# Performance work log

Measured on AMD Instinct MI355X. Metric: run time of the kernel, lower is better.

## Reference

```python
import jax, jax.numpy as jnp
import numpy as np

OUT, IN = 4096, 4096
GROUP_SIZE = 64
NUM_GROUPS = IN // GROUP_SIZE  # 64


def dequantize(packed, mn, scale):
    # packed: [OUT, NUM_GROUPS, GROUP_SIZE//2] int32, byte values 0..255.
    # 4-bit asymmetric layout (torch compress): high nibble holds the first
    # half of each group, low nibble the second half.
    hi = (packed >> 4) & 0xF                      # [OUT, G, 32]
    lo = packed & 0xF                             # [OUT, G, 32]
    vals = jnp.concatenate([hi, lo], axis=-1).astype(jnp.float32)  # [OUT, G, 64]
    w = vals / scale + mn                         # scale, mn broadcast [OUT, G, 1]
    return w.reshape(OUT, IN)


def setup_inputs() -> dict:
    key = jax.random.key(0)
    k1, k2, k3, k4, k5 = jax.random.split(key, 5)
    x = jax.random.normal(k1, (4, 2048, IN), dtype=jnp.float32)
    packed = jax.random.randint(k2, (OUT, NUM_GROUPS, GROUP_SIZE // 2), 0, 256, dtype=jnp.int32)
    mn = jax.random.normal(k3, (OUT, NUM_GROUPS, 1), dtype=jnp.float32) * 0.02
    # scale = B / (mx - mn) is positive; keep it away from zero.
    scale = jax.random.uniform(k4, (OUT, NUM_GROUPS, 1), dtype=jnp.float32) * 200.0 + 100.0
    bias = jax.random.normal(k5, (OUT,), dtype=jnp.float32) * 0.02
    return {"x": x, "packed": packed, "mn": mn, "scale": scale, "bias": bias}


def reference(x, packed, mn, scale, bias):
    w = dequantize(packed, mn, scale)             # [OUT, IN] fp32
    # F.linear: out = x @ w.T + bias
    return jnp.einsum('bsk,nk->bsn', x, w) + bias
```

## Files before the change

kernel.cpp:

```cpp
#include <hip/hip_runtime.h>

typedef unsigned short u16;
typedef unsigned int u32;
typedef _Float16 f16;
typedef f16 f16x2 __attribute__((ext_vector_type(2)));
typedef f16 f16x8 __attribute__((ext_vector_type(8)));
typedef __fp16 h16x2 __attribute__((ext_vector_type(2)));
typedef float f32x4 __attribute__((ext_vector_type(4)));

#define M_DIM 8192
#define N_DIM 4096
#define K_DIM 4096

#define XCVT_BLOCKS 16384
#define W4_BLOCKS 8192
#define IM_BLOCKS 1024

__global__ __launch_bounds__(256) void prep_kernel(
    const float4* __restrict__ x, uint4* __restrict__ xh,
    const int* __restrict__ packed, u32* __restrict__ w4,
    const float* __restrict__ mn, const float* __restrict__ scale,
    uint2* __restrict__ invmn) {
  int b = blockIdx.x;
  if (b < XCVT_BLOCKS) {
    int i = b * 256 + threadIdx.x;
    float4 a0 = x[2 * i], a1 = x[2 * i + 1];
    h16x2 h0 = __builtin_amdgcn_cvt_pkrtz(a0.x, a0.y);
    h16x2 h1 = __builtin_amdgcn_cvt_pkrtz(a0.z, a0.w);
    h16x2 h2 = __builtin_amdgcn_cvt_pkrtz(a1.x, a1.y);
    h16x2 h3 = __builtin_amdgcn_cvt_pkrtz(a1.z, a1.w);
    uint4 o;
    o.x = __builtin_bit_cast(u32, h0);
    o.y = __builtin_bit_cast(u32, h1);
    o.z = __builtin_bit_cast(u32, h2);
    o.w = __builtin_bit_cast(u32, h3);
    xh[i] = o;
  } else if (b < XCVT_BLOCKS + W4_BLOCKS) {
    int idx = (b - XCVT_BLOCKS) * 256 + threadIdx.x;
    int n = idx >> 9, w = idx & 511;
    int g = w >> 3;
    int jb = (w & 7) << 3;
    int sh = (jb < 32) ? 4 : 0;
    const int* p = packed + n * 2048 + g * 32 + (jb & 31);
    u32 out = 0;
#pragma unroll
    for (int t = 0; t < 8; t++) {
      u32 nib = ((u32)p[t] >> sh) & 0xFu;
      int pos = ((t & 1) ? 16 : 0) + ((t >> 1) << 2);
      out |= nib << pos;
    }
    w4[idx] = out;
  } else {
    int idx = (b - XCVT_BLOCKS - W4_BLOCKS) * 256 + threadIdx.x;
    int n = idx & 4095, g = idx >> 12;
    float sc = scale[n * 64 + g];
    float m = mn[n * 64 + g];
    f16 invh = (f16)(1.0f / sc);
    f16 mnh = (f16)(m - 16.0f * (float)invh);
    u32 ib = (u32)__builtin_bit_cast(u16, invh);
    u32 mb = (u32)__builtin_bit_cast(u16, mnh);
    uint2 o;
    o.x = ib | (ib << 16);
    o.y = mb | (mb << 16);
    invmn[idx] = o;
  }
}

__device__ __forceinline__ void gload_lds16(const void* g, void* l) {
  __builtin_amdgcn_global_load_lds(
      (const __attribute__((address_space(1))) void*)g,
      (__attribute__((address_space(3))) void*)l, 16, 0, 0);
}

__global__ __launch_bounds__(256, 2) void gemm4_kernel(
    const u16* __restrict__ A,
    const u32* __restrict__ B4,
    const uint2* __restrict__ IM,
    const float* __restrict__ bias, float* __restrict__ C) {
  __shared__ alignas(16) u16 As[2][256 * 32];
  __shared__ alignas(16) u32 Bs[2][128 * 4];

  const int tid = threadIdx.x;
  const int wave = tid >> 6, lane = tid & 63;
  const int lr = lane & 15, lq = lane >> 4;
  const int bn = blockIdx.x & 31, bm = blockIdx.x >> 5;
  const int m0 = bm << 8, n0 = bn << 7;
  const int wm = (wave & 1) << 7, wn = (wave >> 1) << 6;

  const u16* pA =
      A + (size_t)(m0 + (wave << 6) + (lane >> 2)) * K_DIM + ((lane & 3) << 3);
  char* dstA = (char*)(&As[0][0]) + wave * 4096 + lane * 16;
  const u32* pB = B4 + (size_t)(n0 + ((wave & 1) << 6) + lane) * 512 +
                  ((wave >> 1) << 2);
  char* dstB = (char*)(&Bs[0][0]) + wave * 1024 + lane * 16;
  const uint2* pI = IM + n0 + wn + lr;

  f32x4 acc[8][4] = {};

  for (int kk = 0; kk < 64; ++kk) {
    uint2 im[4];
    const uint2* pIt = pI + kk * 4096;
#pragma unroll
    for (int j = 0; j < 4; j++) im[j] = pIt[j * 16];

#pragma unroll
    for (int s = 0; s < 2; s++)
#pragma unroll
      for (int c = 0; c < 4; c++)
        gload_lds16(pA + kk * 64 + s * 32 + (size_t)c * 16 * K_DIM,
                    dstA + s * 16384 + c * 1024);
    gload_lds16(pB + kk * 8, dstB);
    __syncthreads();

#pragma unroll
    for (int s = 0; s < 2; s++) {
      f16x8 af[8];
#pragma unroll
      for (int i = 0; i < 8; i++)
        af[i] = *(const f16x8*)((const char*)(&As[0][0]) + s * 16384 +
                                (wm + i * 16 + lr) * 64 + lq * 16);
      u32 braw[4];
#pragma unroll
      for (int j = 0; j < 4; j++) braw[j] = Bs[s][(wn + j * 16 + lr) * 4 + lq];

      f16x8 bf[4];
#pragma unroll
      for (int j = 0; j < 4; j++) {
        u32 d = braw[j];
        u32 q0 = ((d << 6) & 0x03C003C0u) | 0x4C004C00u;
        u32 q1 = ((d << 2) & 0x03C003C0u) | 0x4C004C00u;
        u32 q2 = ((d >> 2) & 0x03C003C0u) | 0x4C004C00u;
        u32 q3 = ((d >> 6) & 0x03C003C0u) | 0x4C004C00u;
        f16x2 inv2 = __builtin_bit_cast(f16x2, im[j].x);
        f16x2 mn2 = __builtin_bit_cast(f16x2, im[j].y);
        f16x2 w0 = __builtin_elementwise_fma(__builtin_bit_cast(f16x2, q0), inv2, mn2);
        f16x2 w1 = __builtin_elementwise_fma(__builtin_bit_cast(f16x2, q1), inv2, mn2);
        f16x2 w2 = __builtin_elementwise_fma(__builtin_bit_cast(f16x2, q2), inv2, mn2);
        f16x2 w3 = __builtin_elementwise_fma(__builtin_bit_cast(f16x2, q3), inv2, mn2);
        union {
          f16x8 v;
          u32 d[4];
        } u;
        u.d[0] = __builtin_bit_cast(u32, w0);
        u.d[1] = __builtin_bit_cast(u32, w1);
        u.d[2] = __builtin_bit_cast(u32, w2);
        u.d[3] = __builtin_bit_cast(u32, w3);
        bf[j] = u.v;
      }
#pragma unroll
      for (int i = 0; i < 8; i++)
#pragma unroll
        for (int j = 0; j < 4; j++)
          acc[i][j] = __builtin_amdgcn_mfma_f32_16x16x32_f16(af[i], bf[j],
                                                             acc[i][j], 0, 0, 0);
    }
    __syncthreads();
  }

#pragma unroll
  for (int j = 0; j < 4; j++) {
    int n = n0 + wn + j * 16 + lr;
    float bv = bias[n];
#pragma unroll
    for (int i = 0; i < 8; i++) {
      int mb = m0 + wm + i * 16 + (lq << 2);
#pragma unroll
      for (int t = 0; t < 4; t++)
        C[(size_t)(mb + t) * N_DIM + n] = acc[i][j][t] + bv;
    }
  }
}

__global__ __launch_bounds__(256) void fallback_gemm(
    const float* __restrict__ x, const int* __restrict__ packed,
    const float* __restrict__ mn, const float* __restrict__ scale,
    const float* __restrict__ bias, float* __restrict__ out) {
  __shared__ float As[16][17];
  __shared__ float Bs[16][17];
  int tx = threadIdx.x & 15, ty = threadIdx.x >> 4;
  int m = blockIdx.y * 16 + ty;
  int n = blockIdx.x * 16 + tx;
  float acc = 0.f;
  for (int k0 = 0; k0 < K_DIM; k0 += 16) {
    As[ty][tx] = x[(size_t)m * K_DIM + k0 + tx];
    int nn = blockIdx.x * 16 + ty;
    int k = k0 + tx;
    int g = k >> 6, pos = k & 63;
    int p = packed[nn * 2048 + g * 32 + (pos & 31)];
    int v = (pos < 32) ? ((p >> 4) & 0xF) : (p & 0xF);
    Bs[ty][tx] = (float)v / scale[nn * 64 + g] + mn[nn * 64 + g];
    __syncthreads();
#pragma unroll
    for (int kk = 0; kk < 16; kk++) acc += As[ty][kk] * Bs[tx][kk];
    __syncthreads();
  }
  out[(size_t)m * N_DIM + n] = acc + bias[n];
}

extern "C" void kernel_launch(void* const* d_in, const int* in_sizes, int n_in,
                              void* d_out, int out_size, void* d_ws,
                              size_t ws_size, hipStream_t stream) {
  const float* x = (const float*)d_in[0];
  const int* packed = (const int*)d_in[1];
  const float* mn = (const float*)d_in[2];
  const float* scale = (const float*)d_in[3];
  const float* bias = (const float*)d_in[4];
  float* out = (float*)d_out;

  const size_t offW4 = (size_t)M_DIM * K_DIM * 2;
  const size_t offIM = offW4 + (size_t)N_DIM * K_DIM / 2;
  const size_t need = offIM + (size_t)64 * N_DIM * 8;

  if (ws_size >= need) {
    u16* Xh = (u16*)d_ws;
    u32* W4 = (u32*)((char*)d_ws + offW4);
    uint2* IMp = (uint2*)((char*)d_ws + offIM);
    prep_kernel<<<XCVT_BLOCKS + W4_BLOCKS + IM_BLOCKS, 256, 0, stream>>>(
        (const float4*)x, (uint4*)Xh, packed, W4, mn, scale, IMp);
    gemm4_kernel<<<(M_DIM / 256) * (N_DIM / 128), 256, 0, stream>>>(
        Xh, W4, IMp, bias, out);
  } else {
    dim3 grid(N_DIM / 16, M_DIM / 16);
    fallback_gemm<<<grid, 256, 0, stream>>>(x, packed, mn, scale, bias, out);
  }
}
```

Measured before the change: 515.8 us.

## Double-buffer LDS tiles with prefetch and XOR-swizzle A layout

Converts the GEMM main loop to a double-buffered scheme: the next K-slice of A, B and the scale/min pairs is loaded into the alternate LDS buffer while the current one feeds MFMAs, leaving one barrier per iteration. It also XOR-swizzles the 16-byte chunks of A in LDS to reduce bank conflicts on fragment reads. The trade-off is doubled LDS usage, which may pressure occupancy, plus extra registers for the prefetched scale data.

```diff
diff --git a/kernel.cpp b/kernel.cpp
--- a/kernel.cpp
+++ b/kernel.cpp
@@ -77,8 +77,8 @@
     const u32* __restrict__ B4,
     const uint2* __restrict__ IM,
     const float* __restrict__ bias, float* __restrict__ C) {
-  __shared__ alignas(16) u16 As[2][256 * 32];
-  __shared__ alignas(16) u32 Bs[2][128 * 4];
+  __shared__ alignas(16) u16 As[2][2][256 * 32];
+  __shared__ alignas(16) u32 Bs[2][2][128 * 4];
 
   const int tid = threadIdx.x;
   const int wave = tid >> 6, lane = tid & 63;
@@ -87,41 +87,60 @@
   const int m0 = bm << 8, n0 = bn << 7;
   const int wm = (wave & 1) << 7, wn = (wave >> 1) << 6;
 
+  const int chunkg = (lane & 3) ^ ((lane >> 3) & 3);
   const u16* pA =
-      A + (size_t)(m0 + (wave << 6) + (lane >> 2)) * K_DIM + ((lane & 3) << 3);
-  char* dstA = (char*)(&As[0][0]) + wave * 4096 + lane * 16;
+      A + (size_t)(m0 + (wave << 6) + (lane >> 2)) * K_DIM + (chunkg << 3);
+  char* dstA = (char*)(&As[0][0][0]) + wave * 4096 + lane * 16;
   const u32* pB = B4 + (size_t)(n0 + ((wave & 1) << 6) + lane) * 512 +
                   ((wave >> 1) << 2);
-  char* dstB = (char*)(&Bs[0][0]) + wave * 1024 + lane * 16;
+  char* dstB = (char*)(&Bs[0][0][0]) + wave * 1024 + lane * 16;
   const uint2* pI = IM + n0 + wn + lr;
+  const int aswz = (lq ^ ((lr >> 1) & 3)) << 4;
 
   f32x4 acc[8][4] = {};
 
+#pragma unroll
+  for (int s = 0; s < 2; s++)
+#pragma unroll
+    for (int c = 0; c < 4; c++)
+      gload_lds16(pA + s * 32 + (size_t)c * 16 * K_DIM,
+                  dstA + s * 16384 + c * 1024);
+  gload_lds16(pB, dstB);
+  uint2 imc[4];
+#pragma unroll
+  for (int j = 0; j < 4; j++) imc[j] = pI[j * 16];
+  __syncthreads();
+
+#pragma unroll 2
   for (int kk = 0; kk < 64; ++kk) {
-    uint2 im[4];
-    const uint2* pIt = pI + kk * 4096;
-#pragma unroll
-    for (int j = 0; j < 4; j++) im[j] = pIt[j * 16];
-
-#pragma unroll
-    for (int s = 0; s < 2; s++)
-#pragma unroll
-      for (int c = 0; c < 4; c++)
-        gload_lds16(pA + kk * 64 + s * 32 + (size_t)c * 16 * K_DIM,
-                    dstA + s * 16384 + c * 1024);
-    gload_lds16(pB + kk * 8, dstB);
-    __syncthreads();
-
+    const int buf = kk & 1;
+    uint2 imn[4];
+    if (kk < 63) {
+      const int nb = buf ^ 1;
+#pragma unroll
+      for (int s = 0; s < 2; s++)
+#pragma unroll
+        for (int c = 0; c < 4; c++)
+          gload_lds16(pA + (kk + 1) * 64 + s * 32 + (size_t)c * 16 * K_DIM,
+                      dstA + nb * 32768 + s * 16384 + c * 1024);
+      gload_lds16(pB + (kk + 1) * 8, dstB + nb * 4096);
+#pragma unroll
+      for (int j = 0; j < 4; j++) imn[j] = pI[(kk + 1) * 4096 + j * 16];
+    }
+
+    const char* aB = (const char*)(&As[0][0][0]) + buf * 32768;
+    const char* bB = (const char*)(&Bs[0][0][0]) + buf * 4096;
 #pragma unroll
     for (int s = 0; s < 2; s++) {
       f16x8 af[8];
 #pragma unroll
       for (int i = 0; i < 8; i++)
-        af[i] = *(const f16x8*)((const char*)(&As[0][0]) + s * 16384 +
-                                (wm + i * 16 + lr) * 64 + lq * 16);
+        af[i] = *(const f16x8*)(aB + s * 16384 + (wm + i * 16 + lr) * 64 + aswz);
       u32 braw[4];
 #pragma unroll
-      for (int j = 0; j < 4; j++) braw[j] = Bs[s][(wn + j * 16 + lr) * 4 + lq];
+      for (int j = 0; j < 4; j++)
+        braw[j] =
+            *(const u32*)(bB + s * 2048 + (((wn + j * 16 + lr) << 2) + lq) * 4);
 
       f16x8 bf[4];
 #pragma unroll
@@ -131,8 +150,8 @@
         u32 q1 = ((d << 2) & 0x03C003C0u) | 0x4C004C00u;
         u32 q2 = ((d >> 2) & 0x03C003C0u) | 0x4C004C00u;
         u32 q3 = ((d >> 6) & 0x03C003C0u) | 0x4C004C00u;
-        f16x2 inv2 = __builtin_bit_cast(f16x2, im[j].x);
-        f16x2 mn2 = __builtin_bit_cast(f16x2, im[j].y);
+        f16x2 inv2 = __builtin_bit_cast(f16x2, imc[j].x);
+        f16x2 mn2 = __builtin_bit_cast(f16x2, imc[j].y);
         f16x2 w0 = __builtin_elementwise_fma(__builtin_bit_cast(f16x2, q0), inv2, mn2);
         f16x2 w1 = __builtin_elementwise_fma(__builtin_bit_cast(f16x2, q1), inv2, mn2);
         f16x2 w2 = __builtin_elementwise_fma(__builtin_bit_cast(f16x2, q2), inv2, mn2);
@@ -155,6 +174,10 @@
                                                              acc[i][j], 0, 0, 0);
     }
     __syncthreads();
+    if (kk < 63) {
+#pragma unroll
+      for (int j = 0; j < 4; j++) imc[j] = imn[j];
+    }
   }
 
 #pragma unroll
```

Result: no change. 523.8 us (+1.5%).

## Use 256x256 tiles, 512 threads, triple-buffered LDS pipeline and swizzled A layout

Applied to the files above, without the earlier changes.

Enlarges the GEMM block tile to 256x256 with 8 waves. The K loop becomes a 3-stage asynchronous global-to-LDS pipeline with explicit vmcnt waits, so loads for later K-steps overlap MFMA work on the current one. The A tile is XOR-swizzled in LDS to cut bank conflicts, and the per-group scale/min values are now staged through LDS instead of loaded directly from global memory. Compute is split into four phases with barriers and s_setprio. The much larger LDS footprint limits occupancy, and the hand-written waitcnt logic is fragile.

```diff
diff --git a/kernel.cpp b/kernel.cpp
--- a/kernel.cpp
+++ b/kernel.cpp
@@ -71,91 +71,132 @@
       (const __attribute__((address_space(1))) void*)g,
       (__attribute__((address_space(3))) void*)l, 16, 0, 0);
 }
-
-__global__ __launch_bounds__(256, 2) void gemm4_kernel(
+__device__ __forceinline__ void gload_lds4(const void* g, void* l) {
+  __builtin_amdgcn_global_load_lds(
+      (const __attribute__((address_space(1))) void*)g,
+      (__attribute__((address_space(3))) void*)l, 4, 0, 0);
+}
+
+__global__ __launch_bounds__(512, 2) void gemm4_kernel(
     const u16* __restrict__ A,
     const u32* __restrict__ B4,
     const uint2* __restrict__ IM,
     const float* __restrict__ bias, float* __restrict__ C) {
-  __shared__ alignas(16) u16 As[2][256 * 32];
-  __shared__ alignas(16) u32 Bs[2][128 * 4];
+  __shared__ alignas(16) u16 As[3][256 * 64];
+  __shared__ alignas(16) u32 Bs[3][256 * 8];
+  __shared__ alignas(16) uint2 Is[3][256];
 
   const int tid = threadIdx.x;
   const int wave = tid >> 6, lane = tid & 63;
   const int lr = lane & 15, lq = lane >> 4;
-  const int bn = blockIdx.x & 31, bm = blockIdx.x >> 5;
-  const int m0 = bm << 8, n0 = bn << 7;
+  const int bn = blockIdx.x & 15, bm = blockIdx.x >> 4;
+  const int m0 = bm << 8, n0 = bn << 8;
   const int wm = (wave & 1) << 7, wn = (wave >> 1) << 6;
 
-  const u16* pA =
-      A + (size_t)(m0 + (wave << 6) + (lane >> 2)) * K_DIM + ((lane & 3) << 3);
-  char* dstA = (char*)(&As[0][0]) + wave * 4096 + lane * 16;
-  const u32* pB = B4 + (size_t)(n0 + ((wave & 1) << 6) + lane) * 512 +
-                  ((wave >> 1) << 2);
-  char* dstB = (char*)(&Bs[0][0]) + wave * 1024 + lane * 16;
-  const uint2* pI = IM + n0 + wn + lr;
+  const int cgA = (tid & 7) ^ ((tid >> 3) & 7);
+  const u16* pA = A + (size_t)(m0 + (tid >> 3)) * K_DIM + (cgA << 3);
+  const u32* pB = B4 + (size_t)(n0 + (tid >> 1)) * 512 + ((tid & 1) << 2);
+  const u32* pIg = (const u32*)IM + (size_t)(n0 + (tid >> 1)) * 2 + (tid & 1);
+
+#define STAGE(tt, ss)                                                       \
+  do {                                                                      \
+    char* dA_ = (char*)(&As[(ss)][0]) + (tid << 4);                         \
+    char* dB_ = (char*)(&Bs[(ss)][0]) + (tid << 4);                         \
+    char* dI_ = (char*)(&Is[(ss)][0]) + (tid << 2);                         \
+    _Pragma("unroll") for (int p_ = 0; p_ < 4; p_++)                        \
+        gload_lds16(pA + (tt) * 64 + (size_t)p_ * 64 * K_DIM,               \
+                    dA_ + p_ * 8192);                                       \
+    gload_lds16(pB + (tt) * 8, dB_);                                        \
+    gload_lds4(pIg + (size_t)(tt) * 8192, dI_);                             \
+  } while (0)
 
   f32x4 acc[8][4] = {};
 
-  for (int kk = 0; kk < 64; ++kk) {
-    uint2 im[4];
-    const uint2* pIt = pI + kk * 4096;
-#pragma unroll
-    for (int j = 0; j < 4; j++) im[j] = pIt[j * 16];
-
-#pragma unroll
-    for (int s = 0; s < 2; s++)
-#pragma unroll
-      for (int c = 0; c < 4; c++)
-        gload_lds16(pA + kk * 64 + s * 32 + (size_t)c * 16 * K_DIM,
-                    dstA + s * 16384 + c * 1024);
-    gload_lds16(pB + kk * 8, dstB);
-    __syncthreads();
-
-#pragma unroll
-    for (int s = 0; s < 2; s++) {
-      f16x8 af[8];
-#pragma unroll
-      for (int i = 0; i < 8; i++)
-        af[i] = *(const f16x8*)((const char*)(&As[0][0]) + s * 16384 +
-                                (wm + i * 16 + lr) * 64 + lq * 16);
-      u32 braw[4];
-#pragma unroll
-      for (int j = 0; j < 4; j++) braw[j] = Bs[s][(wn + j * 16 + lr) * 4 + lq];
-
-      f16x8 bf[4];
-#pragma unroll
-      for (int j = 0; j < 4; j++) {
-        u32 d = braw[j];
-        u32 q0 = ((d << 6) & 0x03C003C0u) | 0x4C004C00u;
-        u32 q1 = ((d << 2) & 0x03C003C0u) | 0x4C004C00u;
-        u32 q2 = ((d >> 2) & 0x03C003C0u) | 0x4C004C00u;
-        u32 q3 = ((d >> 6) & 0x03C003C0u) | 0x4C004C00u;
-        f16x2 inv2 = __builtin_bit_cast(f16x2, im[j].x);
-        f16x2 mn2 = __builtin_bit_cast(f16x2, im[j].y);
-        f16x2 w0 = __builtin_elementwise_fma(__builtin_bit_cast(f16x2, q0), inv2, mn2);
-        f16x2 w1 = __builtin_elementwise_fma(__builtin_bit_cast(f16x2, q1), inv2, mn2);
-        f16x2 w2 = __builtin_elementwise_fma(__builtin_bit_cast(f16x2, q2), inv2, mn2);
-        f16x2 w3 = __builtin_elementwise_fma(__builtin_bit_cast(f16x2, q3), inv2, mn2);
-        union {
-          f16x8 v;
-          u32 d[4];
-        } u;
-        u.d[0] = __builtin_bit_cast(u32, w0);
-        u.d[1] = __builtin_bit_cast(u32, w1);
-        u.d[2] = __builtin_bit_cast(u32, w2);
-        u.d[3] = __builtin_bit_cast(u32, w3);
-        bf[j] = u.v;
-      }
-#pragma unroll
-      for (int i = 0; i < 8; i++)
-#pragma unroll
-        for (int j = 0; j < 4; j++)
-          acc[i][j] = __builtin_amdgcn_mfma_f32_16x16x32_f16(af[i], bf[j],
-                                                             acc[i][j], 0, 0, 0);
-    }
-    __syncthreads();
-  }
+  STAGE(0, 0);
+  STAGE(1, 1);
+  STAGE(2, 2);
+  asm volatile("s_waitcnt vmcnt(12)" ::: "memory");
+  __builtin_amdgcn_s_barrier();
+
+  int cur = 0;
+
+#define PHASE(mh, nh)                                                         \
+  do {                                                                        \
+    f16x8 af[4][2];                                                           \
+    _Pragma("unroll") for (int ii = 0; ii < 4; ii++)                          \
+        _Pragma("unroll") for (int ks = 0; ks < 2; ks++) {                    \
+      int row_ = wm + ((mh)*4 + ii) * 16 + lr;                                \
+      int ch_ = ((ks << 2) + lq) ^ (lr & 7);                                  \
+      af[ii][ks] = *(const f16x8*)((const char*)(&As[cur][0]) + row_ * 128 +  \
+                                   (ch_ << 4));                               \
+    }                                                                         \
+    u32 braw[2][2];                                                           \
+    uint2 imv[2];                                                             \
+    _Pragma("unroll") for (int jj = 0; jj < 2; jj++) {                        \
+      int rowb_ = wn + ((nh)*2 + jj) * 16 + lr;                               \
+      imv[jj] = Is[cur][rowb_];                                               \
+      _Pragma("unroll") for (int ks = 0; ks < 2; ks++)                        \
+          braw[jj][ks] = Bs[cur][rowb_ * 8 + (ks << 2) + lq];                 \
+    }                                                                         \
+    __builtin_amdgcn_s_barrier();                                             \
+    asm volatile("s_waitcnt lgkmcnt(0)" ::: "memory");                        \
+    __builtin_amdgcn_sched_barrier(0);                                        \
+    __builtin_amdgcn_s_setprio(1);                                            \
+    f16x8 bf[2][2];                                                           \
+    _Pragma("unroll") for (int jj = 0; jj < 2; jj++) {                        \
+      f16x2 inv2 = __builtin_bit_cast(f16x2, imv[jj].x);                      \
+      f16x2 mn2 = __builtin_bit_cast(f16x2, imv[jj].y);                       \
+      _Pragma("unroll") for (int ks = 0; ks < 2; ks++) {                      \
+        u32 d_ = braw[jj][ks];                                                \
+        u32 q0 = ((d_ << 6) & 0x03C003C0u) | 0x4C004C00u;                     \
+        u32 q1 = ((d_ << 2) & 0x03C003C0u) | 0x4C004C00u;                     \
+        u32 q2 = ((d_ >> 2) & 0x03C003C0u) | 0x4C004C00u;                     \
+        u32 q3 = ((d_ >> 6) & 0x03C003C0u) | 0x4C004C00u;                     \
+        f16x2 w0 =                                                            \
+            __builtin_elementwise_fma(__builtin_bit_cast(f16x2, q0), inv2, mn2); \
+        f16x2 w1 =                                                            \
+            __builtin_elementwise_fma(__builtin_bit_cast(f16x2, q1), inv2, mn2); \
+        f16x2 w2 =                                                            \
+            __builtin_elementwise_fma(__builtin_bit_cast(f16x2, q2), inv2, mn2); \
+        f16x2 w3 =                                                            \
+            __builtin_elementwise_fma(__builtin_bit_cast(f16x2, q3), inv2, mn2); \
+        union {                                                               \
+          f16x8 v;                                                            \
+          u32 d[4];                                                           \
+        } u_;                                                                 \
+        u_.d[0] = __builtin_bit_cast(u32, w0);                                \
+        u_.d[1] = __builtin_bit_cast(u32, w1);                                \
+        u_.d[2] = __builtin_bit_cast(u32, w2);                                \
+        u_.d[3] = __builtin_bit_cast(u32, w3);                                \
+        bf[jj][ks] = u_.v;                                                    \
+      }                                                                       \
+    }                                                                         \
+    _Pragma("unroll") for (int ii = 0; ii < 4; ii++)                          \
+        _Pragma("unroll") for (int jj = 0; jj < 2; jj++)                      \
+            _Pragma("unroll") for (int ks = 0; ks < 2; ks++)                  \
+        acc[(mh)*4 + ii][(nh)*2 + jj] =                                       \
+            __builtin_amdgcn_mfma_f32_16x16x32_f16(                           \
+                af[ii][ks], bf[jj][ks], acc[(mh)*4 + ii][(nh)*2 + jj], 0, 0,  \
+                0);                                                           \
+    __builtin_amdgcn_s_setprio(0);                                            \
+  } while (0)
+
+#pragma unroll 1
+  for (int t = 0; t < 64; ++t) {
+    PHASE(0, 0);
+    PHASE(1, 0);
+    PHASE(0, 1);
+    PHASE(1, 1);
+    if (t < 62)
+      asm volatile("s_waitcnt vmcnt(6)" ::: "memory");
+    else
+      asm volatile("s_waitcnt vmcnt(0)" ::: "memory");
+    __builtin_amdgcn_s_barrier();
+    if (t < 61) STAGE(t + 3, cur);
+    cur = (cur == 2) ? 0 : cur + 1;
+  }
+#undef PHASE
+#undef STAGE
 
 #pragma unroll
   for (int j = 0; j < 4; j++) {
@@ -217,7 +258,7 @@
     uint2* IMp = (uint2*)((char*)d_ws + offIM);
     prep_kernel<<<XCVT_BLOCKS + W4_BLOCKS + IM_BLOCKS, 256, 0, stream>>>(
         (const float4*)x, (uint4*)Xh, packed, W4, mn, scale, IMp);
-    gemm4_kernel<<<(M_DIM / 256) * (N_DIM / 128), 256, 0, stream>>>(
+    gemm4_kernel<<<(M_DIM / 256) * (N_DIM / 256), 512, 0, stream>>>(
         Xh, W4, IMp, bias, out);
   } else {
     dim3 grid(N_DIM / 16, M_DIM / 16);
```

New measurement: 621.5 us. 20.5% more time.

## Restructure GEMM into 256x256 tiles with triple-buffered async LDS pipeline

Applied to the files above, without the earlier changes.

The GEMM now uses 512-thread blocks computing 256x256 output tiles with a 64-wide K step and a three-stage global-to-LDS prefetch pipeline driven by manual vmcnt waits. The A tile in LDS is XOR-swizzled, the packed weights are re-laid out group-major, and scale/min values are staged through LDS. Blocks are remapped across XCDs, and MFMA phases are bracketed with setprio. The aim is to hide memory latency and increase reuse per tile. The cost is much more LDS per block, which lowers occupancy, and fragile hand-written waitcnt logic.

```diff
diff --git a/kernel.cpp b/kernel.cpp
--- a/kernel.cpp
+++ b/kernel.cpp
@@ -49,7 +49,7 @@
       int pos = ((t & 1) ? 16 : 0) + ((t >> 1) << 2);
       out |= nib << pos;
     }
-    w4[idx] = out;
+    w4[g * 32768 + n * 8 + (w & 7)] = out;
   } else {
     int idx = (b - XCVT_BLOCKS - W4_BLOCKS) * 256 + threadIdx.x;
     int n = idx & 4095, g = idx >> 12;
@@ -71,91 +71,155 @@
       (const __attribute__((address_space(1))) void*)g,
       (__attribute__((address_space(3))) void*)l, 16, 0, 0);
 }
-
-__global__ __launch_bounds__(256, 2) void gemm4_kernel(
+__device__ __forceinline__ void gload_lds4(const void* g, void* l) {
+  __builtin_amdgcn_global_load_lds(
+      (const __attribute__((address_space(1))) void*)g,
+      (__attribute__((address_space(3))) void*)l, 4, 0, 0);
+}
+
+__global__ __launch_bounds__(512, 2) void gemm4_kernel(
     const u16* __restrict__ A,
     const u32* __restrict__ B4,
     const uint2* __restrict__ IM,
     const float* __restrict__ bias, float* __restrict__ C) {
-  __shared__ alignas(16) u16 As[2][256 * 32];
-  __shared__ alignas(16) u32 Bs[2][128 * 4];
+  __shared__ alignas(16) u16 As[3][256 * 64];
+  __shared__ alignas(16) u32 Bs[3][2][256][4];
+  __shared__ alignas(16) uint2 Is[3][256];
 
   const int tid = threadIdx.x;
   const int wave = tid >> 6, lane = tid & 63;
   const int lr = lane & 15, lq = lane >> 4;
-  const int bn = blockIdx.x & 31, bm = blockIdx.x >> 5;
-  const int m0 = bm << 8, n0 = bn << 7;
+  const int wg = ((int)blockIdx.x & 7) * 64 + ((int)blockIdx.x >> 3);
+  const int bn = wg & 15, bm = wg >> 4;
+  const int m0 = bm << 8, n0 = bn << 8;
   const int wm = (wave & 1) << 7, wn = (wave >> 1) << 6;
 
-  const u16* pA =
-      A + (size_t)(m0 + (wave << 6) + (lane >> 2)) * K_DIM + ((lane & 3) << 3);
-  char* dstA = (char*)(&As[0][0]) + wave * 4096 + lane * 16;
-  const u32* pB = B4 + (size_t)(n0 + ((wave & 1) << 6) + lane) * 512 +
-                  ((wave >> 1) << 2);
-  char* dstB = (char*)(&Bs[0][0]) + wave * 1024 + lane * 16;
-  const uint2* pI = IM + n0 + wn + lr;
+  const int cgA = (tid & 7) ^ ((tid >> 3) & 7);
+  const u16* pA = A + (size_t)(m0 + (tid >> 3)) * K_DIM + (cgA << 3);
+  const u32* pB = B4 + (size_t)(n0 + (tid & 255)) * 8 + ((tid >> 8) << 2);
+  const u32* pIg = (const u32*)IM + (size_t)(n0 + (tid >> 1)) * 2 + (tid & 1);
+
+#define STAGE(tt, ss)                                                     \
+  do {                                                                    \
+    char* dA_ = (char*)(&As[(ss)][0]) + (tid << 4);                       \
+    char* dB_ = (char*)(&Bs[(ss)][0][0][0]) + (tid << 4);                 \
+    char* dI_ = (char*)(&Is[(ss)][0]) + (tid << 2);                       \
+    _Pragma("unroll") for (int p_ = 0; p_ < 4; p_++)                      \
+        gload_lds16(pA + (tt) * 64 + (size_t)p_ * 64 * K_DIM,             \
+                    dA_ + p_ * 8192);                                     \
+    gload_lds16(pB + (size_t)(tt) * 32768, dB_);                          \
+    gload_lds4(pIg + (size_t)(tt) * 8192, dI_);                           \
+  } while (0)
 
   f32x4 acc[8][4] = {};
 
-  for (int kk = 0; kk < 64; ++kk) {
-    uint2 im[4];
-    const uint2* pIt = pI + kk * 4096;
-#pragma unroll
-    for (int j = 0; j < 4; j++) im[j] = pIt[j * 16];
-
-#pragma unroll
-    for (int s = 0; s < 2; s++)
-#pragma unroll
-      for (int c = 0; c < 4; c++)
-        gload_lds16(pA + kk * 64 + s * 32 + (size_t)c * 16 * K_DIM,
-                    dstA + s * 16384 + c * 1024);
-    gload_lds16(pB + kk * 8, dstB);
-    __syncthreads();
-
-#pragma unroll
-    for (int s = 0; s < 2; s++) {
-      f16x8 af[8];
-#pragma unroll
-      for (int i = 0; i < 8; i++)
-        af[i] = *(const f16x8*)((const char*)(&As[0][0]) + s * 16384 +
-                                (wm + i * 16 + lr) * 64 + lq * 16);
-      u32 braw[4];
-#pragma unroll
-      for (int j = 0; j < 4; j++) braw[j] = Bs[s][(wn + j * 16 + lr) * 4 + lq];
-
-      f16x8 bf[4];
-#pragma unroll
-      for (int j = 0; j < 4; j++) {
-        u32 d = braw[j];
-        u32 q0 = ((d << 6) & 0x03C003C0u) | 0x4C004C00u;
-        u32 q1 = ((d << 2) & 0x03C003C0u) | 0x4C004C00u;
-        u32 q2 = ((d >> 2) & 0x03C003C0u) | 0x4C004C00u;
-        u32 q3 = ((d >> 6) & 0x03C003C0u) | 0x4C004C00u;
-        f16x2 inv2 = __builtin_bit_cast(f16x2, im[j].x);
-        f16x2 mn2 = __builtin_bit_cast(f16x2, im[j].y);
-        f16x2 w0 = __builtin_elementwise_fma(__builtin_bit_cast(f16x2, q0), inv2, mn2);
-        f16x2 w1 = __builtin_elementwise_fma(__builtin_bit_cast(f16x2, q1), inv2, mn2);
-        f16x2 w2 = __builtin_elementwise_fma(__builtin_bit_cast(f16x2, q2), inv2, mn2);
-        f16x2 w3 = __builtin_elementwise_fma(__builtin_bit_cast(f16x2, q3), inv2, mn2);
+  STAGE(0, 0);
+  STAGE(1, 1);
+  STAGE(2, 2);
+  asm volatile("s_waitcnt vmcnt(12)" ::: "memory");
+  __builtin_amdgcn_s_barrier();
+
+  int cur = 0;
+
+#pragma unroll 1
+  for (int t = 0; t < 64; ++t) {
+    const char* aB = (const char*)(&As[cur][0]);
+
+    uint2 isv[4];
+    u32 braw[4][2];
+    f16x8 af[4][2];
+#pragma unroll
+    for (int j = 0; j < 4; j++) {
+      int rowb = wn + j * 16 + lr;
+      isv[j] = Is[cur][rowb];
+#pragma unroll
+      for (int ks = 0; ks < 2; ks++) braw[j][ks] = Bs[cur][ks][rowb][lq];
+    }
+#pragma unroll
+    for (int ii = 0; ii < 4; ii++)
+#pragma unroll
+      for (int ks = 0; ks < 2; ks++) {
+        int row_ = wm + ii * 16 + lr;
+        int ch_ = ((ks << 2) + lq) ^ (lr & 7);
+        af[ii][ks] = *(const f16x8*)(aB + row_ * 128 + (ch_ << 4));
+      }
+    __builtin_amdgcn_s_barrier();
+    asm volatile("s_waitcnt lgkmcnt(0)" ::: "memory");
+    __builtin_amdgcn_sched_barrier(0);
+    __builtin_amdgcn_s_setprio(1);
+    f16x8 bf[4][2];
+#pragma unroll
+    for (int j = 0; j < 4; j++) {
+      f16x2 inv2 = __builtin_bit_cast(f16x2, isv[j].x);
+      f16x2 mn2 = __builtin_bit_cast(f16x2, isv[j].y);
+#pragma unroll
+      for (int ks = 0; ks < 2; ks++) {
+        u32 d_ = braw[j][ks];
+        u32 q0 = ((d_ << 6) & 0x03C003C0u) | 0x4C004C00u;
+        u32 q1 = ((d_ << 2) & 0x03C003C0u) | 0x4C004C00u;
+        u32 q2 = ((d_ >> 2) & 0x03C003C0u) | 0x4C004C00u;
+        u32 q3 = ((d_ >> 6) & 0x03C003C0u) | 0x4C004C00u;
+        f16x2 w0 =
+            __builtin_elementwise_fma(__builtin_bit_cast(f16x2, q0), inv2, mn2);
+        f16x2 w1 =
+            __builtin_elementwise_fma(__builtin_bit_cast(f16x2, q1), inv2, mn2);
+        f16x2 w2 =
+            __builtin_elementwise_fma(__builtin_bit_cast(f16x2, q2), inv2, mn2);
+        f16x2 w3 =
+            __builtin_elementwise_fma(__builtin_bit_cast(f16x2, q3), inv2, mn2);
         union {
           f16x8 v;
           u32 d[4];
-        } u;
-        u.d[0] = __builtin_bit_cast(u32, w0);
-        u.d[1] = __builtin_bit_cast(u32, w1);
-        u.d[2] = __builtin_bit_cast(u32, w2);
-        u.d[3] = __builtin_bit_cast(u32, w3);
-        bf[j] = u.v;
+        } u_;
+        u_.d[0] = __builtin_bit_cast(u32, w0);
+        u_.d[1] = __builtin_bit_cast(u32, w1);
+        u_.d[2] = __builtin_bit_cast(u32, w2);
+        u_.d[3] = __builtin_bit_cast(u32, w3);
+        bf[j][ks] = u_.v;
       }
-#pragma unroll
-      for (int i = 0; i < 8; i++)
-#pragma unroll
-        for (int j = 0; j < 4; j++)
-          acc[i][j] = __builtin_amdgcn_mfma_f32_16x16x32_f16(af[i], bf[j],
-                                                             acc[i][j], 0, 0, 0);
-    }
-    __syncthreads();
-  }
+    }
+#pragma unroll
+    for (int ii = 0; ii < 4; ii++)
+#pragma unroll
+      for (int j = 0; j < 4; j++)
+#pragma unroll
+        for (int ks = 0; ks < 2; ks++)
+          acc[ii][j] = __builtin_amdgcn_mfma_f32_16x16x32_f16(
+              af[ii][ks], bf[j][ks], acc[ii][j], 0, 0, 0);
+    __builtin_amdgcn_s_setprio(0);
+
+    f16x8 ag[4][2];
+#pragma unroll
+    for (int ii = 0; ii < 4; ii++)
+#pragma unroll
+      for (int ks = 0; ks < 2; ks++) {
+        int row_ = wm + 64 + ii * 16 + lr;
+        int ch_ = ((ks << 2) + lq) ^ (lr & 7);
+        ag[ii][ks] = *(const f16x8*)(aB + row_ * 128 + (ch_ << 4));
+      }
+    __builtin_amdgcn_s_barrier();
+    asm volatile("s_waitcnt lgkmcnt(0)" ::: "memory");
+    __builtin_amdgcn_sched_barrier(0);
+    __builtin_amdgcn_s_setprio(1);
+#pragma unroll
+    for (int ii = 0; ii < 4; ii++)
+#pragma unroll
+      for (int j = 0; j < 4; j++)
+#pragma unroll
+        for (int ks = 0; ks < 2; ks++)
+          acc[4 + ii][j] = __builtin_amdgcn_mfma_f32_16x16x32_f16(
+              ag[ii][ks], bf[j][ks], acc[4 + ii][j], 0, 0, 0);
+    __builtin_amdgcn_s_setprio(0);
+
+    if (t < 62)
+      asm volatile("s_waitcnt vmcnt(6)" ::: "memory");
+    else
+      asm volatile("s_waitcnt vmcnt(0)" ::: "memory");
+    __builtin_amdgcn_s_barrier();
+    if (t < 61) STAGE(t + 3, cur);
+    cur = (cur == 2) ? 0 : cur + 1;
+  }
+#undef STAGE
 
 #pragma unroll
   for (int j = 0; j < 4; j++) {
@@ -217,7 +281,7 @@
     uint2* IMp = (uint2*)((char*)d_ws + offIM);
     prep_kernel<<<XCVT_BLOCKS + W4_BLOCKS + IM_BLOCKS, 256, 0, stream>>>(
         (const float4*)x, (uint4*)Xh, packed, W4, mn, scale, IMp);
-    gemm4_kernel<<<(M_DIM / 256) * (N_DIM / 128), 256, 0, stream>>>(
+    gemm4_kernel<<<(M_DIM / 256) * (N_DIM / 256), 512, 0, stream>>>(
         Xh, W4, IMp, bias, out);
   } else {
     dim3 grid(N_DIM / 16, M_DIM / 16);
```

Measured after the change: 582.3 us. 1.13x slower.
